# Kernel tuning notes

Hardware: AMD Instinct MI355X
Metric: run time of the kernel (lower is better)

Reference implementation:

```python
import jax, jax.numpy as jnp
import numpy as np
import math

HID = 300   # model dim (d_k in the source's scale factor)
HDIM = 64   # attention projection dim
NH = 8      # heads = last axis of view(B,S,HDIM//8,8)
DH = HDIM // NH
L = 6


def pos_encoding(S, d):
    pos = jnp.arange(S, dtype=jnp.float32)[:, None]
    i = jnp.arange(d)
    expo = jnp.where(i % 2 == 0, i, i - 1).astype(jnp.float32) / d
    ang = pos / jnp.power(jnp.float32(10000.0), expo)  # (S, d)
    return jnp.where(i % 2 == 0, jnp.sin(ang), jnp.cos(ang))


def norm(x, g, b):
    mu = jnp.mean(x, axis=-1, keepdims=True)
    var = jnp.var(x, axis=-1, keepdims=True, ddof=1)  # torch.var is unbiased
    return g * (x - mu) / jnp.sqrt(var + 1e-8) + b


def mha(x, mask, wq, wk, wv, wo):
    B, S, _ = x.shape
    # view(B,S,DH,NH).permute(3,0,1,2): head h = feature indices i*NH+h
    q = (x @ wq).reshape(B, S, DH, NH).transpose(3, 0, 1, 2)  # (NH,B,S,DH)
    k = (x @ wk).reshape(B, S, DH, NH).transpose(3, 0, 1, 2)
    v = (x @ wv).reshape(B, S, DH, NH).transpose(3, 0, 1, 2)
    e = jnp.einsum('hbqd,hbkd->hbqk', q, k) / math.sqrt(HID)
    e = jnp.where(mask[None], jnp.float32(-1e9), e)
    alpha = jax.nn.softmax(e, axis=-1)
    h = jnp.einsum('hbqk,hbkd->hbqd', alpha, v)
    # cat(head0..head7, dim=2) -> head-major feature layout
    a = h.transpose(1, 2, 0, 3).reshape(B, S, HDIM)
    return a @ wo


def encoder(x, mask, wq, wk, wv, wo, w1, bb1, w2, bb2, g1, be1, g2, be2):
    x2 = mha(x, mask, wq, wk, wv, wo)
    x = norm(x2 + x, g1, be1)
    ff = jnp.maximum(x @ w1 + bb1, 0.0) @ w2 + bb2
    x = norm(ff + x, g2, be2)
    return x


def setup_inputs() -> dict:
    key = jax.random.key(0)
    ks = jax.random.split(key, 16)
    B, S, V, C = 32, 512, 50000, 1000
    sc = 0.02
    return {
        'x': jax.random.randint(ks[0], (B, S), 0, V),
        'emb': jax.random.normal(ks[1], (V, HID), jnp.float32) * sc,
        'WQ': jax.random.normal(ks[2], (L, HID, HDIM), jnp.float32) * sc,
        'WK': jax.random.normal(ks[3], (L, HID, HDIM), jnp.float32) * sc,
        'WV': jax.random.normal(ks[4], (L, HID, HDIM), jnp.float32) * sc,
        'WO': jax.random.normal(ks[5], (L, HDIM, HID), jnp.float32) * sc,
        'W1': jax.random.normal(ks[6], (L, HID, 4 * HID), jnp.float32) * sc,
        'b1': jax.random.normal(ks[7], (L, 4 * HID), jnp.float32) * sc,
        'W2': jax.random.normal(ks[8], (L, 4 * HID, HID), jnp.float32) * sc,
        'b2': jax.random.normal(ks[9], (L, HID), jnp.float32) * sc,
        'gamma1': jnp.ones((L,), jnp.float32),
        'beta1': jnp.zeros((L,), jnp.float32),
        'gamma2': jnp.ones((L,), jnp.float32),
        'beta2': jnp.zeros((L,), jnp.float32),
        'V_d': jax.random.normal(ks[10], (HID, C), jnp.float32) * sc,
        'gamma_f': jnp.float32(1.0),
        'beta_f': jnp.float32(0.0),
    }


def reference(x, emb, WQ, WK, WV, WO, W1, b1, W2, b2,
              gamma1, beta1, gamma2, beta2, V_d, gamma_f, beta_f):
    B, S = x.shape
    mask = (x == 0)[:, None, :] * jnp.ones((1, S, 1), bool)  # (B,S,S)
    x1 = emb[x]                               # (B,S,HID)
    x2 = x1 + pos_encoding(S, HID)[None]
    acc = x2 + x1                             # dense residual running sum
    out = x2
    for l in range(L):
        out = encoder(acc, mask, WQ[l], WK[l], WV[l], WO[l],
                      W1[l], b1[l], W2[l], b2[l],
                      gamma1[l], beta1[l], gamma2[l], beta2[l])
        acc = acc + out
    logits = jnp.sum(out, axis=1) @ V_d       # (B,C)
    return jax.nn.softmax(norm(logits, gamma_f, beta_f), axis=1)
```

## Files before the change

### kernel.cpp

```cpp
#include <hip/hip_runtime.h>
#include <hip/hip_bf16.h>
#include <cstdio>
#include <cstdint>

#define BATCH 32
#define SEQ 512
#define BSQ (BATCH*SEQ)
#define HIDD 300
#define HD 64
#define NHEAD 8
#define DHEAD 8
#define NLAYERS 6
#define FFD 1200
#define NCLS 1000
#define NSPLIT 4
#define KCH (SEQ/NSPLIT)
#define CLS_KS 4
#define CLS_KC (HIDD/CLS_KS)

typedef short short8 __attribute__((ext_vector_type(8)));
typedef float floatx4 __attribute__((ext_vector_type(4)));

__device__ __forceinline__ short f2b(float v){
  __hip_bfloat16 h = __float2bfloat16(v);
  short s; __builtin_memcpy(&s, &h, 2); return s;
}
__device__ __forceinline__ unsigned pk2(float a, float b){
  return (unsigned)(unsigned short)f2b(a) | ((unsigned)(unsigned short)f2b(b) << 16);
}

#define ASYNC16(g, l) __builtin_amdgcn_global_load_lds( \
  (const __attribute__((address_space(1))) unsigned int*)(g), \
  (__attribute__((address_space(3))) unsigned int*)(l), 16, 0, 0)

__global__ void t10_embed(const int* __restrict__ toks,
                          const float* __restrict__ emb,
                          float* __restrict__ acc,
                          short* __restrict__ accbf){
  int idx = blockIdx.x*256 + threadIdx.x;
  if (idx >= BSQ*320) return;
  int row = idx / 320;
  int j   = idx - row*320;
  if (j >= HIDD){ accbf[(size_t)row*320 + j] = 0; return; }
  int t = toks[row];
  float e = emb[(size_t)t*HIDD + j];
  int s = row & (SEQ-1);
  float expo = (float)(j & ~1) * (1.0f/(float)HIDD);
  float ang  = (float)s * expf(-expo * 9.210340371976184f);
  float pe   = (j & 1) ? cosf(ang) : sinf(ang);
  float v = 2.0f*e + pe;
  acc[(size_t)row*HIDD + j] = v;
  accbf[(size_t)row*320 + j] = f2b(v);
}

__global__ void prep_w(const float* __restrict__ src, short* __restrict__ dst,
                       int K, int N, int Kpad, int rows, int nbase,
                       int sls, int dls, int total, int perm){
  int idx = blockIdx.x*256 + threadIdx.x;
  if (idx >= total) return;
  int l   = idx / (rows*Kpad);
  int rem = idx - l*(rows*Kpad);
  int n = rem / Kpad;
  int k = rem - n*Kpad;
  int sc = perm ? ((n & 7)*8 + (n >> 3)) : n;
  float v = (n < N && k < K) ? src[(size_t)l*sls + (size_t)k*N + sc] : 0.f;
  dst[(size_t)l*dls + (size_t)(nbase+n)*Kpad + k] = f2b(v);
}

__global__ __launch_bounds__(256) void mm128(
    const short* __restrict__ A, const short* __restrict__ Wt,
    const float* __restrict__ bias, float* __restrict__ C,
    short* __restrict__ Cb,
    int M, int N, int Kpad, int Npad, int nnb, int relu){
  __shared__ short sA[128][32];
  __shared__ short sB[128][32];
  int wg = blockIdx.x;
  int cpx = gridDim.x >> 3;
  int swz = (wg & 7)*cpx + (wg >> 3);
  int mt = swz / nnb, nt = swz - mt*nnb;
  int m0 = mt*128, n0 = nt*128;
  int tid = threadIdx.x;
  int lane = tid & 63, wv = tid >> 6;
  int wm = (wv & 1)*64, wn = (wv >> 1)*64;
  int l15 = lane & 15, quad = lane >> 4;
  floatx4 acc[4][4] = {};
  int lr = tid >> 2, lc = (tid & 3)*8;
  const short* Ab = A  + (size_t)(m0 + lr)*Kpad + lc;
  const short* Bb = Wt + (size_t)(n0 + lr)*Kpad + lc;
  char* sAb = (char*)sA + wv*1024;
  char* sBb = (char*)sB + wv*1024;
  int nch = Kpad >> 5;
  for (int c = 0; c < nch; c++){
    int k0 = c*32;
    __syncthreads();
    ASYNC16(Ab + k0,                    sAb);
    ASYNC16(Ab + (size_t)64*Kpad + k0,  sAb + 4096);
    ASYNC16(Bb + k0,                    sBb);
    ASYNC16(Bb + (size_t)64*Kpad + k0,  sBb + 4096);
    __syncthreads();
    short8 af[4], bfr[4];
    #pragma unroll
    for (int i=0;i<4;i++)
      af[i] = *(const short8*)&sA[wm + i*16 + l15][quad*8];
    #pragma unroll
    for (int j=0;j<4;j++)
      bfr[j] = *(const short8*)&sB[wn + j*16 + l15][quad*8];
    #pragma unroll
    for (int i=0;i<4;i++)
      #pragma unroll
      for (int j=0;j<4;j++)
        acc[i][j] = __builtin_amdgcn_mfma_f32_16x16x32_bf16(af[i], bfr[j], acc[i][j], 0,0,0);
  }
  if (Cb){
    #pragma unroll
    for (int j=0;j<4;j++){
      int n = n0 + wn + j*16 + l15;
      float bv = (bias && n < N) ? bias[n] : 0.f;
      #pragma unroll
      for (int i=0;i<4;i++){
        int mbase = m0 + wm + i*16 + quad*4;
        #pragma unroll
        for (int r=0;r<4;r++){
          float cv = acc[i][j][r] + bv;
          if (relu) cv = fmaxf(cv, 0.f);
          Cb[(size_t)(mbase+r)*Npad + n] = (n < N) ? f2b(cv) : (short)0;
        }
      }
    }
  } else {
    #pragma unroll
    for (int j=0;j<4;j++){
      int n = n0 + wn + j*16 + l15;
      if (n >= N) continue;
      float bv = bias ? bias[n] : 0.f;
      #pragma unroll
      for (int i=0;i<4;i++){
        int mbase = m0 + wm + i*16 + quad*4;
        #pragma unroll
        for (int r=0;r<4;r++){
          float cv = acc[i][j][r] + bv;
          if (relu) cv = fmaxf(cv, 0.f);
          C[(size_t)(mbase+r)*N + n] = cv;
        }
      }
    }
  }
}

__global__ __launch_bounds__(256) void t14_attn(
    const float* __restrict__ qkv, const int* __restrict__ toks,
    float* __restrict__ pp, float* __restrict__ ps){
  __shared__ float kb[KCH][9];
  __shared__ float vb[KCH][9];
  __shared__ float msk[KCH];
  __shared__ short Pl[4][16][136];
  int blk = blockIdx.x;
  int ks = blk & (NSPLIT-1);
  int bh = blk >> 2;
  int b = bh >> 3, h = bh & 7;
  int tid = threadIdx.x;
  int lane = tid & 63, w = tid >> 6;
  int quad = lane >> 4, l15 = lane & 15;
  int kbase = ks*KCH;
  {
    int r = tid >> 1, half = (tid & 1)*4;
    const float* src = qkv + (size_t)(b*SEQ + kbase + r)*192 + h*8 + half;
    float4 kx = *(const float4*)(src + 64);
    float4 vx = *(const float4*)(src + 128);
    kb[r][half+0]=kx.x; kb[r][half+1]=kx.y; kb[r][half+2]=kx.z; kb[r][half+3]=kx.w;
    vb[r][half+0]=vx.x; vb[r][half+1]=vx.y; vb[r][half+2]=vx.z; vb[r][half+3]=vx.w;
  }
  if (tid < KCH)
    msk[tid] = (toks[b*SEQ + kbase + tid]==0) ? -1e9f : 0.f;
  __syncthreads();

  short8 kfrag[8];
  #pragma unroll
  for (int kt=0;kt<8;kt++){
    short8 f;
    #pragma unroll
    for (int j=0;j<8;j++) f[j] = 0;
    if (quad == 0){
      #pragma unroll
      for (int j=0;j<8;j++) f[j] = f2b(kb[kt*16 + l15][j]);
    }
    kfrag[kt] = f;
  }
  short8 vfrag[4];
  #pragma unroll
  for (int ks2=0;ks2<4;ks2++){
    short8 f;
    #pragma unroll
    for (int j=0;j<8;j++) f[j] = 0;
    if (l15 < 8){
      #pragma unroll
      for (int j=0;j<8;j++) f[j] = f2b(vb[ks2*32 + quad*8 + j][l15]);
    } else if (l15 == 8){
      #pragma unroll
      for (int j=0;j<8;j++) f[j] = (short)0x3F80;
    }
    vfrag[ks2] = f;
  }
  const float scale = 0.057735026918962574f;

  for (int t = 0; t < 8; t++){
    int q0 = w*128 + t*16;
    short8 qf;
    #pragma unroll
    for (int j=0;j<8;j++) qf[j] = 0;
    if (quad == 0){
      const float* qsrc = qkv + (size_t)(b*SEQ + q0 + l15)*192 + h*8;
      float4 a = *(const float4*)qsrc;
      float4 c = *(const float4*)(qsrc + 4);
      qf[0]=f2b(a.x*scale); qf[1]=f2b(a.y*scale); qf[2]=f2b(a.z*scale); qf[3]=f2b(a.w*scale);
      qf[4]=f2b(c.x*scale); qf[5]=f2b(c.y*scale); qf[6]=f2b(c.z*scale); qf[7]=f2b(c.w*scale);
    }
    #pragma unroll
    for (int kt2 = 0; kt2 < 4; kt2++){
      floatx4 z = {0.f,0.f,0.f,0.f};
      floatx4 a0 = __builtin_amdgcn_mfma_f32_16x16x32_bf16(kfrag[2*kt2],   qf, z, 0,0,0);
      floatx4 a1 = __builtin_amdgcn_mfma_f32_16x16x32_bf16(kfrag[2*kt2+1], qf, z, 0,0,0);
      float p0[4], p1[4];
      #pragma unroll
      for (int r=0;r<4;r++){
        float m0 = msk[(2*kt2)*16   + quad*4 + r];
        float m1 = msk[(2*kt2+1)*16 + quad*4 + r];
        p0[r] = __expf(fminf(a0[r] + m0, 60.f));
        p1[r] = __expf(fminf(a1[r] + m1, 60.f));
      }
      uint2 u0, u1;
      u0.x = pk2(p0[0], p0[1]); u0.y = pk2(p0[2], p0[3]);
      u1.x = pk2(p1[0], p1[1]); u1.y = pk2(p1[2], p1[3]);
      *(uint2*)&Pl[w][l15][(2*kt2)*16   + quad*4] = u0;
      *(uint2*)&Pl[w][l15][(2*kt2+1)*16 + quad*4] = u1;
    }
    floatx4 o = {0.f,0.f,0.f,0.f};
    #pragma unroll
    for (int ks2=0; ks2<4; ks2++){
      short8 pa = *(const short8*)&Pl[w][l15][ks2*32 + quad*8];
      o = __builtin_amdgcn_mfma_f32_16x16x32_bf16(pa, vfrag[ks2], o, 0,0,0);
    }
    if (l15 < 8){
      #pragma unroll
      for (int r=0;r<4;r++){
        int q = q0 + quad*4 + r;
        pp[(size_t)ks*BSQ*64 + (size_t)(b*SEQ+q)*64 + h*8 + l15] = o[r];
      }
    } else if (l15 == 8){
      #pragma unroll
      for (int r=0;r<4;r++){
        int q = q0 + quad*4 + r;
        ps[(size_t)ks*BSQ*8 + (size_t)(b*SEQ+q)*8 + h] = o[r];
      }
    }
  }
}

__global__ __launch_bounds__(256) void t12_attn_comb(
    const float* __restrict__ pp, const float* __restrict__ ps,
    short* __restrict__ aout){
  int idx = blockIdx.x*256 + threadIdx.x;
  if (idx >= BSQ*8) return;
  float s = 0.f;
  for (int k=0;k<NSPLIT;k++) s += ps[(size_t)k*BSQ*8 + idx];
  float inv = 1.f/s;
  int bsq = idx >> 3, h = idx & 7;
  size_t base = (size_t)bsq*64 + h*8;
  float o[8] = {};
  for (int k=0;k<NSPLIT;k++){
    const float4* p = (const float4*)(pp + (size_t)k*BSQ*64 + base);
    float4 a = p[0], bq = p[1];
    o[0]+=a.x; o[1]+=a.y; o[2]+=a.z; o[3]+=a.w;
    o[4]+=bq.x; o[5]+=bq.y; o[6]+=bq.z; o[7]+=bq.w;
  }
  short8 r;
  for (int d=0;d<8;d++) r[d] = f2b(o[d]*inv);
  *(short8*)(aout + base) = r;
}

__global__ __launch_bounds__(256) void t10_addnorm(
                 const float* __restrict__ xa, const float* __restrict__ xb,
                 float* __restrict__ y, short* __restrict__ ybf,
                 float* __restrict__ accum, short* __restrict__ accbf,
                 const float* __restrict__ gamma, const float* __restrict__ beta,
                 int l){
  __shared__ float red[8];
  int row = blockIdx.x, tid = threadIdx.x;
  size_t base = (size_t)row*HIDD;
  size_t bbase = (size_t)row*320;
  float v0 = xa[base+tid] + xb[base+tid];
  float v1 = 0.f;
  int has1 = (tid+256 < HIDD);
  if (has1) v1 = xa[base+tid+256] + xb[base+tid+256];
  float s = v0+v1, sq = v0*v0+v1*v1;
  for (int off=32; off; off>>=1){ s += __shfl_down(s,off); sq += __shfl_down(sq,off); }
  int lane = tid & 63, w = tid >> 6;
  if (lane==0){ red[w]=s; red[4+w]=sq; }
  __syncthreads();
  float sum = red[0]+red[1]+red[2]+red[3];
  float ssq = red[4]+red[5]+red[6]+red[7];
  float mu  = sum * (1.0f/HIDD);
  float var = (ssq - (float)HIDD*mu*mu) * (1.0f/(HIDD-1));
  float rstd = rsqrtf(var + 1e-8f);
  float g = gamma[l], be = beta[l];
  float o0 = g*(v0-mu)*rstd + be;
  y[base+tid] = o0;
  if (ybf) ybf[bbase+tid] = f2b(o0);
  if (accum){
    float a0 = accum[base+tid] + o0;
    accum[base+tid] = a0;
    if (accbf) accbf[bbase+tid] = f2b(a0);
  }
  if (has1){
    float o1 = g*(v1-mu)*rstd + be;
    y[base+tid+256] = o1;
    if (ybf) ybf[bbase+tid+256] = f2b(o1);
    if (accum){
      float a1 = accum[base+tid+256] + o1;
      accum[base+tid+256] = a1;
      if (accbf) accbf[bbase+tid+256] = f2b(a1);
    }
  } else if (tid+256 < 320){
    if (ybf) ybf[bbase+tid+256] = 0;
    if (accbf) accbf[bbase+tid+256] = 0;
  }
}

__global__ __launch_bounds__(256) void t13_colsum_part(
    const float* __restrict__ outb, float* __restrict__ part){
  int blk = blockIdx.x;
  int b = blk >> 3, c = blk & 7;
  int tid = threadIdx.x;
  size_t base = (size_t)b*SEQ*HIDD + (size_t)c*64*HIDD;
  int j1 = tid + 256;
  float s0 = 0.f, s1 = 0.f;
  for (int t = 0; t < 64; t++){
    const float* row = outb + base + (size_t)t*HIDD;
    s0 += row[tid];
    if (j1 < HIDD) s1 += row[j1];
  }
  float* dst = part + (size_t)(c*BATCH + b)*HIDD;
  dst[tid] = s0;
  if (j1 < HIDD) dst[j1] = s1;
}

__global__ void t13_colsum_comb(const float* __restrict__ part,
                                float* __restrict__ sums){
  int idx = blockIdx.x*256 + threadIdx.x;
  if (idx >= BATCH*HIDD) return;
  float s = 0.f;
  for (int c = 0; c < 8; c++) s += part[(size_t)c*BATCH*HIDD + idx];
  sums[idx] = s;
}

__global__ __launch_bounds__(256) void t13_cls(
    const float* __restrict__ sums, const float* __restrict__ W,
    float* __restrict__ plog){
  int gid = blockIdx.x*256 + threadIdx.x;
  if (gid >= CLS_KS*BATCH*NCLS) return;
  int c = gid / (BATCH*NCLS);
  int rem = gid - c*(BATCH*NCLS);
  int m = rem / NCLS, n = rem - m*NCLS;
  const float* arow = sums + m*HIDD + c*CLS_KC;
  const float* wcol = W + (size_t)c*CLS_KC*NCLS + n;
  float acc = 0.f;
  #pragma unroll 5
  for (int k = 0; k < CLS_KC; k++)
    acc = fmaf(arow[k], wcol[(size_t)k*NCLS], acc);
  plog[gid] = acc;
}

__device__ __forceinline__ float t10_bsum(float val, float* red){
  for (int off=32; off; off>>=1) val += __shfl_down(val, off);
  __syncthreads();
  if ((threadIdx.x & 63)==0) red[threadIdx.x>>6] = val;
  __syncthreads();
  return red[0]+red[1]+red[2]+red[3];
}
__device__ __forceinline__ float t10_bmax(float val, float* red){
  for (int off=32; off; off>>=1) val = fmaxf(val, __shfl_down(val, off));
  __syncthreads();
  if ((threadIdx.x & 63)==0) red[threadIdx.x>>6] = val;
  __syncthreads();
  return fmaxf(fmaxf(red[0],red[1]), fmaxf(red[2],red[3]));
}

__global__ __launch_bounds__(256) void t10_final(
                  const float* __restrict__ plog,
                  const float* __restrict__ gf, const float* __restrict__ bff,
                  float* __restrict__ outp){
  __shared__ float red[4];
  int b = blockIdx.x, tid = threadIdx.x;
  size_t base = (size_t)b*NCLS;
  float v[4];
  float s = 0.f, sq = 0.f;
  for (int t=0;t<4;t++){
    int j = tid + t*256;
    float x = 0.f;
    if (j < NCLS){
      for (int c=0;c<CLS_KS;c++) x += plog[(size_t)c*BATCH*NCLS + base + j];
    }
    v[t] = x; s += x; sq += x*x;
  }
  s  = t10_bsum(s, red);
  sq = t10_bsum(sq, red);
  float mu  = s * (1.0f/NCLS);
  float var = (sq - (float)NCLS*mu*mu) * (1.0f/(NCLS-1));
  float rstd = rsqrtf(var + 1e-8f);
  float g = gf[0], be = bff[0];
  float y[4]; float mx = -1e30f;
  for (int t=0;t<4;t++){
    int j = tid + t*256;
    y[t] = g*(v[t]-mu)*rstd + be;
    if (j < NCLS) mx = fmaxf(mx, y[t]);
  }
  mx = t10_bmax(mx, red);
  float p[4]; float es = 0.f;
  for (int t=0;t<4;t++){
    int j = tid + t*256;
    p[t] = (j < NCLS) ? __expf(y[t]-mx) : 0.f;
    es += p[t];
  }
  es = t10_bsum(es, red);
  float inv = 1.0f/es;
  for (int t=0;t<4;t++){
    int j = tid + t*256;
    if (j < NCLS) outp[base+j] = p[t]*inv;
  }
}

extern "C" void kernel_launch(void* const* d_in, const int* in_sizes, int n_in,
                              void* d_out, int out_size, void* d_ws, size_t ws_size,
                              hipStream_t stream){
  const int*   toks = (const int*)d_in[0];
  const float* emb  = (const float*)d_in[1];
  const float* WQ   = (const float*)d_in[2];
  const float* WK   = (const float*)d_in[3];
  const float* WV   = (const float*)d_in[4];
  const float* WO   = (const float*)d_in[5];
  const float* W1   = (const float*)d_in[6];
  const float* b1   = (const float*)d_in[7];
  const float* W2   = (const float*)d_in[8];
  const float* b2   = (const float*)d_in[9];
  const float* g1   = (const float*)d_in[10];
  const float* be1  = (const float*)d_in[11];
  const float* g2   = (const float*)d_in[12];
  const float* be2  = (const float*)d_in[13];
  const float* Vd   = (const float*)d_in[14];
  const float* gf   = (const float*)d_in[15];
  const float* bff  = (const float*)d_in[16];
  float* outp = (float*)d_out;

  float* acc    = (float*)d_ws;
  float* xn     = acc    + (size_t)BSQ*HIDD;
  float* outb   = xn     + (size_t)BSQ*HIDD;
  float* tmp    = outb   + (size_t)BSQ*HIDD;
  float* qkv    = tmp    + (size_t)BSQ*HIDD;
  float* sums   = qkv    + (size_t)BSQ*192;
  float* logits = sums   + BATCH*HIDD;
  float* pp     = tmp;
  float* ps     = tmp + (size_t)NSPLIT*BSQ*64;
  short* acc_bf = (short*)(logits + BATCH*NCLS);
  short* xn_bf  = acc_bf + (size_t)BSQ*320;
  short* aat_bf = xn_bf  + (size_t)BSQ*320;
  short* ff1_bf = aat_bf + (size_t)BSQ*64;
  short* wqkv = ff1_bf + (size_t)BSQ*1280;
  short* wo   = wqkv + (size_t)6*256*320;
  short* w1t  = wo   + (size_t)6*384*64;
  short* w2t  = w1t  + (size_t)6*1280*320;
  float* cspart = (float*)(w2t + (size_t)6*384*1280);
  float* plog   = cspart + (size_t)8*BATCH*HIDD;

  {
    int tq = 6*64*320;
    prep_w<<<(tq+255)/256,256,0,stream>>>(WQ, wqkv, 300, 64, 320, 64, 0,   19200, 81920, tq, 1);
    prep_w<<<(tq+255)/256,256,0,stream>>>(WK, wqkv, 300, 64, 320, 64, 64,  19200, 81920, tq, 1);
    prep_w<<<(tq+255)/256,256,0,stream>>>(WV, wqkv, 300, 64, 320, 64, 128, 19200, 81920, tq, 1);
    prep_w<<<(tq+255)/256,256,0,stream>>>(WQ, wqkv, 300, 0,  320, 64, 192, 19200, 81920, tq, 0);
    int to = 6*384*64;
    prep_w<<<(to+255)/256,256,0,stream>>>(WO, wo, 64, 300, 64, 384, 0, 19200, 24576, to, 0);
    int t1 = 6*1280*320;
    prep_w<<<(t1+255)/256,256,0,stream>>>(W1, w1t, 300, 1200, 320, 1280, 0, 360000, 409600, t1, 0);
    int t2 = 6*384*1280;
    prep_w<<<(t2+255)/256,256,0,stream>>>(W2, w2t, 1200, 300, 1280, 384, 0, 360000, 491520, t2, 0);
  }

  t10_embed<<<(BSQ*320+255)/256, 256, 0, stream>>>(toks, emb, acc, acc_bf);

  for (int l = 0; l < NLAYERS; l++){
    mm128<<<128*2,256,0,stream>>>(acc_bf, wqkv + (size_t)l*81920, nullptr, qkv, nullptr,
                                  BSQ, 192, 320, 0, 2, 0);
    t14_attn<<<BATCH*NHEAD*NSPLIT, 256, 0, stream>>>(qkv, toks, pp, ps);
    t12_attn_comb<<<(BSQ*8)/256, 256, 0, stream>>>(pp, ps, aat_bf);
    mm128<<<128*3,256,0,stream>>>(aat_bf, wo + (size_t)l*24576, nullptr, tmp, nullptr,
                                  BSQ, 300, 64, 0, 3, 0);
    t10_addnorm<<<BSQ,256,0,stream>>>(tmp, acc, xn, xn_bf, nullptr, nullptr, g1, be1, l);
    mm128<<<128*10,256,0,stream>>>(xn_bf, w1t + (size_t)l*409600, b1 + (size_t)l*FFD,
                                   nullptr, ff1_bf, BSQ, 1200, 320, 1280, 10, 1);
    mm128<<<128*3,256,0,stream>>>(ff1_bf, w2t + (size_t)l*491520, b2 + (size_t)l*HIDD,
                                  tmp, nullptr, BSQ, 300, 1280, 0, 3, 0);
    t10_addnorm<<<BSQ,256,0,stream>>>(tmp, xn, outb, nullptr, acc, acc_bf, g2, be2, l);
  }

  t13_colsum_part<<<BATCH*8, 256, 0, stream>>>(outb, cspart);
  t13_colsum_comb<<<(BATCH*HIDD+255)/256, 256, 0, stream>>>(cspart, sums);
  t13_cls<<<(CLS_KS*BATCH*NCLS)/256, 256, 0, stream>>>(sums, Vd, plog);
  t10_final<<<BATCH, 256, 0, stream>>>(plog, gf, bff, outp);

  hipStreamCaptureStatus cs = hipStreamCaptureStatusNone;
  hipStreamIsCapturing(stream, &cs);
  if (cs == hipStreamCaptureStatusNone){
    hipError_t e_sync = hipStreamSynchronize(stream);
    float ho[4] = {-1,-1,-1,-1};
    hipMemcpy(ho, d_out, 16, hipMemcpyDeviceToHost);
    fprintf(stderr, "[t15] sync=%s out[0..3]=%g,%g,%g,%g\n",
            hipGetErrorString(e_sync), ho[0], ho[1], ho[2], ho[3]);
    fflush(stderr);
  }
}
```

Measured before the change: 1.159 ms.

## Replace 128x128 GEMM with smaller padded-LDS tiles and skip unused norm output

```diff
diff --git a/kernel.cpp b/kernel.cpp
--- a/kernel.cpp
+++ b/kernel.cpp
@@ -28,10 +28,6 @@
 __device__ __forceinline__ unsigned pk2(float a, float b){
   return (unsigned)(unsigned short)f2b(a) | ((unsigned)(unsigned short)f2b(b) << 16);
 }
-
-#define ASYNC16(g, l) __builtin_amdgcn_global_load_lds( \
-  (const __attribute__((address_space(1))) unsigned int*)(g), \
-  (__attribute__((address_space(3))) unsigned int*)(l), 16, 0, 0)
 
 __global__ void t10_embed(const int* __restrict__ toks,
                           const float* __restrict__ emb,
@@ -67,58 +63,125 @@
   dst[(size_t)l*dls + (size_t)(nbase+n)*Kpad + k] = f2b(v);
 }
 
-__global__ __launch_bounds__(256) void mm128(
+__global__ __launch_bounds__(256) void mm_a16(
     const short* __restrict__ A, const short* __restrict__ Wt,
     const float* __restrict__ bias, float* __restrict__ C,
     short* __restrict__ Cb,
     int M, int N, int Kpad, int Npad, int nnb, int relu){
-  __shared__ short sA[128][32];
-  __shared__ short sB[128][32];
+  __shared__ short sA[64][40];
+  __shared__ short sB[64][40];
   int wg = blockIdx.x;
   int cpx = gridDim.x >> 3;
   int swz = (wg & 7)*cpx + (wg >> 3);
   int mt = swz / nnb, nt = swz - mt*nnb;
-  int m0 = mt*128, n0 = nt*128;
+  int m0 = mt*64, n0 = nt*64;
   int tid = threadIdx.x;
   int lane = tid & 63, wv = tid >> 6;
-  int wm = (wv & 1)*64, wn = (wv >> 1)*64;
+  int wm = (wv & 1)*32, wn = (wv >> 1)*32;
   int l15 = lane & 15, quad = lane >> 4;
-  floatx4 acc[4][4] = {};
-  int lr = tid >> 2, lc = (tid & 3)*8;
-  const short* Ab = A  + (size_t)(m0 + lr)*Kpad + lc;
-  const short* Bb = Wt + (size_t)(n0 + lr)*Kpad + lc;
-  char* sAb = (char*)sA + wv*1024;
-  char* sBb = (char*)sB + wv*1024;
+  floatx4 acc[2][2] = {};
+  int srow = tid >> 2, sko = (tid & 3)*8;
+  const short* Arow = A  + (size_t)(m0 + srow)*Kpad + sko;
+  const short* Brow = Wt + (size_t)(n0 + srow)*Kpad + sko;
   int nch = Kpad >> 5;
   for (int c = 0; c < nch; c++){
     int k0 = c*32;
     __syncthreads();
-    ASYNC16(Ab + k0,                    sAb);
-    ASYNC16(Ab + (size_t)64*Kpad + k0,  sAb + 4096);
-    ASYNC16(Bb + k0,                    sBb);
-    ASYNC16(Bb + (size_t)64*Kpad + k0,  sBb + 4096);
+    *(short8*)&sA[srow][sko] = *(const short8*)(Arow + k0);
+    *(short8*)&sB[srow][sko] = *(const short8*)(Brow + k0);
     __syncthreads();
-    short8 af[4], bfr[4];
-    #pragma unroll
-    for (int i=0;i<4;i++)
+    short8 af[2], bf[2];
+    for (int i=0;i<2;i++)
       af[i] = *(const short8*)&sA[wm + i*16 + l15][quad*8];
-    #pragma unroll
-    for (int j=0;j<4;j++)
-      bfr[j] = *(const short8*)&sB[wn + j*16 + l15][quad*8];
-    #pragma unroll
-    for (int i=0;i<4;i++)
-      #pragma unroll
-      for (int j=0;j<4;j++)
-        acc[i][j] = __builtin_amdgcn_mfma_f32_16x16x32_bf16(af[i], bfr[j], acc[i][j], 0,0,0);
+    for (int j=0;j<2;j++)
+      bf[j] = *(const short8*)&sB[wn + j*16 + l15][quad*8];
+    for (int i=0;i<2;i++)
+      for (int j=0;j<2;j++)
+        acc[i][j] = __builtin_amdgcn_mfma_f32_16x16x32_bf16(af[i], bf[j], acc[i][j], 0,0,0);
   }
   if (Cb){
-    #pragma unroll
-    for (int j=0;j<4;j++){
+    for (int j=0;j<2;j++){
       int n = n0 + wn + j*16 + l15;
       float bv = (bias && n < N) ? bias[n] : 0.f;
+      for (int i=0;i<2;i++){
+        int mbase = m0 + wm + i*16 + quad*4;
+        for (int r=0;r<4;r++){
+          float cv = acc[i][j][r] + bv;
+          if (relu) cv = fmaxf(cv, 0.f);
+          Cb[(size_t)(mbase+r)*Npad + n] = (n < N) ? f2b(cv) : (short)0;
+        }
+      }
+    }
+  } else {
+    for (int j=0;j<2;j++){
+      int n = n0 + wn + j*16 + l15;
+      if (n >= N) continue;
+      float bv = bias ? bias[n] : 0.f;
+      for (int i=0;i<2;i++){
+        int mbase = m0 + wm + i*16 + quad*4;
+        for (int r=0;r<4;r++){
+          float cv = acc[i][j][r] + bv;
+          if (relu) cv = fmaxf(cv, 0.f);
+          C[(size_t)(mbase+r)*N + n] = cv;
+        }
+      }
+    }
+  }
+}
+
+__global__ __launch_bounds__(256) void mm64(
+    const short* __restrict__ A, const short* __restrict__ Wt,
+    const float* __restrict__ bias, float* __restrict__ C,
+    short* __restrict__ Cb,
+    int M, int N, int Kpad, int Npad, int nnb, int relu){
+  __shared__ short sA[64][40];
+  __shared__ short sB[128][40];
+  int wg = blockIdx.x;
+  int cpx = gridDim.x >> 3;
+  int swz = (wg & 7)*cpx + (wg >> 3);
+  int mt = swz / nnb, nt = swz - mt*nnb;
+  int m0 = mt*64, n0 = nt*128;
+  int tid = threadIdx.x;
+  int lane = tid & 63, wv = tid >> 6;
+  int l15 = lane & 15, quad = lane >> 4;
+  int wn = wv*32;
+  floatx4 acc[4][2] = {};
+  int lr = tid >> 2, lc = (tid & 3)*8;
+  const short* Arow  = A  + (size_t)(m0 + lr)*Kpad + lc;
+  const short* Brow0 = Wt + (size_t)(n0 + lr)*Kpad + lc;
+  const short* Brow1 = Wt + (size_t)(n0 + 64 + lr)*Kpad + lc;
+  int nch = Kpad >> 5;
+  for (int c = 0; c < nch; c++){
+    int k0 = c*32;
+    short8 va  = *(const short8*)(Arow  + k0);
+    short8 vb0 = *(const short8*)(Brow0 + k0);
+    short8 vb1 = *(const short8*)(Brow1 + k0);
+    __syncthreads();
+    *(short8*)&sA[lr][lc]      = va;
+    *(short8*)&sB[lr][lc]      = vb0;
+    *(short8*)&sB[64+lr][lc]   = vb1;
+    __syncthreads();
+    short8 af[4], bf[2];
+    #pragma unroll
+    for (int i=0;i<4;i++)
+      af[i] = *(const short8*)&sA[i*16 + l15][quad*8];
+    #pragma unroll
+    for (int j=0;j<2;j++)
+      bf[j] = *(const short8*)&sB[wn + j*16 + l15][quad*8];
+    #pragma unroll
+    for (int i=0;i<4;i++)
+      #pragma unroll
+      for (int j=0;j<2;j++)
+        acc[i][j] = __builtin_amdgcn_mfma_f32_16x16x32_bf16(af[i], bf[j], acc[i][j], 0,0,0);
+  }
+  if (Cb){
+    #pragma unroll
+    for (int j=0;j<2;j++){
+      int n = n0 + wn + j*16 + l15;
+      float bv = (bias && n < N) ? bias[n] : 0.f;
       #pragma unroll
       for (int i=0;i<4;i++){
-        int mbase = m0 + wm + i*16 + quad*4;
+        int mbase = m0 + i*16 + quad*4;
         #pragma unroll
         for (int r=0;r<4;r++){
           float cv = acc[i][j][r] + bv;
@@ -129,13 +192,13 @@
     }
   } else {
     #pragma unroll
-    for (int j=0;j<4;j++){
+    for (int j=0;j<2;j++){
       int n = n0 + wn + j*16 + l15;
       if (n >= N) continue;
       float bv = bias ? bias[n] : 0.f;
       #pragma unroll
       for (int i=0;i<4;i++){
-        int mbase = m0 + wm + i*16 + quad*4;
+        int mbase = m0 + i*16 + quad*4;
         #pragma unroll
         for (int r=0;r<4;r++){
           float cv = acc[i][j][r] + bv;
@@ -304,7 +367,7 @@
   float rstd = rsqrtf(var + 1e-8f);
   float g = gamma[l], be = beta[l];
   float o0 = g*(v0-mu)*rstd + be;
-  y[base+tid] = o0;
+  if (y) y[base+tid] = o0;
   if (ybf) ybf[bbase+tid] = f2b(o0);
   if (accum){
     float a0 = accum[base+tid] + o0;
@@ -313,7 +376,7 @@
   }
   if (has1){
     float o1 = g*(v1-mu)*rstd + be;
-    y[base+tid+256] = o1;
+    if (y) y[base+tid+256] = o1;
     if (ybf) ybf[bbase+tid+256] = f2b(o1);
     if (accum){
       float a1 = accum[base+tid+256] + o1;
@@ -488,18 +551,19 @@
   t10_embed<<<(BSQ*320+255)/256, 256, 0, stream>>>(toks, emb, acc, acc_bf);
 
   for (int l = 0; l < NLAYERS; l++){
-    mm128<<<128*2,256,0,stream>>>(acc_bf, wqkv + (size_t)l*81920, nullptr, qkv, nullptr,
-                                  BSQ, 192, 320, 0, 2, 0);
+    mm64<<<256*2,256,0,stream>>>(acc_bf, wqkv + (size_t)l*81920, nullptr, qkv, nullptr,
+                                 BSQ, 192, 320, 0, 2, 0);
     t14_attn<<<BATCH*NHEAD*NSPLIT, 256, 0, stream>>>(qkv, toks, pp, ps);
     t12_attn_comb<<<(BSQ*8)/256, 256, 0, stream>>>(pp, ps, aat_bf);
-    mm128<<<128*3,256,0,stream>>>(aat_bf, wo + (size_t)l*24576, nullptr, tmp, nullptr,
-                                  BSQ, 300, 64, 0, 3, 0);
+    mm_a16<<<256*5,256,0,stream>>>(aat_bf, wo + (size_t)l*24576, nullptr, tmp, nullptr,
+                                   BSQ, 300, 64, 0, 5, 0);
     t10_addnorm<<<BSQ,256,0,stream>>>(tmp, acc, xn, xn_bf, nullptr, nullptr, g1, be1, l);
-    mm128<<<128*10,256,0,stream>>>(xn_bf, w1t + (size_t)l*409600, b1 + (size_t)l*FFD,
-                                   nullptr, ff1_bf, BSQ, 1200, 320, 1280, 10, 1);
-    mm128<<<128*3,256,0,stream>>>(ff1_bf, w2t + (size_t)l*491520, b2 + (size_t)l*HIDD,
-                                  tmp, nullptr, BSQ, 300, 1280, 0, 3, 0);
-    t10_addnorm<<<BSQ,256,0,stream>>>(tmp, xn, outb, nullptr, acc, acc_bf, g2, be2, l);
+    mm64<<<256*10,256,0,stream>>>(xn_bf, w1t + (size_t)l*409600, b1 + (size_t)l*FFD,
+                                  nullptr, ff1_bf, BSQ, 1200, 320, 1280, 10, 1);
+    mm64<<<256*3,256,0,stream>>>(ff1_bf, w2t + (size_t)l*491520, b2 + (size_t)l*HIDD,
+                                 tmp, nullptr, BSQ, 300, 1280, 0, 3, 0);
+    t10_addnorm<<<BSQ,256,0,stream>>>(tmp, xn, (l==NLAYERS-1)?outb:nullptr, nullptr,
+                                      acc, acc_bf, g2, be2, l);
   }
 
   t13_colsum_part<<<BATCH*8, 256, 0, stream>>>(outb, cspart);
@@ -513,7 +577,7 @@
     hipError_t e_sync = hipStreamSynchronize(stream);
     float ho[4] = {-1,-1,-1,-1};
     hipMemcpy(ho, d_out, 16, hipMemcpyDeviceToHost);
-    fprintf(stderr, "[t15] sync=%s out[0..3]=%g,%g,%g,%g\n",
+    fprintf(stderr, "[t16] sync=%s out[0..3]=%g,%g,%g,%g\n",
             hipGetErrorString(e_sync), ho[0], ho[1], ho[2], ho[3]);
     fflush(stderr);
   }
```

Result: faster. 1.123 ms (-3.1%).
